# Kernel tuning notes

Measured on AMD Instinct MI355X. Metric: run time of the kernel, lower is better.

## Reference

```python
import jax, jax.numpy as jnp
import numpy as np
from jax import lax

B, T, D, H, V = 64, 512, 256, 1024, 32000


def setup_inputs() -> dict:
    key = jax.random.key(0)
    kx, kw, ku, kd = jax.random.split(key, 4)
    s_in = 1.0 / np.sqrt(D)
    s_h = 1.0 / np.sqrt(H)
    return {
        "x": jax.random.normal(kx, (B, T, D), dtype=jnp.float32),
        "W": jax.random.normal(kw, (D, H), dtype=jnp.float32) * s_in,
        "U": jax.random.normal(ku, (H, H), dtype=jnp.float32) * s_h,
        "b": jnp.zeros((H,), dtype=jnp.float32),
        "Wd": jax.random.normal(kd, (H, V), dtype=jnp.float32) * s_h,
        "bd": jnp.zeros((V,), dtype=jnp.float32),
    }


def reference(x, W, U, b, Wd, bd):
    # Precompute input projection for all timesteps: [B,T,H]
    xW = jnp.einsum("btd,dh->bth", x, W) + b

    def step(h, xw_t):
        # SimpleRNNCell: h_t = tanh(x_t W + b + h_{t-1} U)
        h_new = jnp.tanh(xw_t + h @ U)
        return h_new, None

    h0 = jnp.zeros((x.shape[0], U.shape[0]), dtype=x.dtype)
    hT, _ = lax.scan(step, h0, jnp.swapaxes(xW, 0, 1))  # scan over T

    logits = hT @ Wd + bd  # [B, V]
    return jax.nn.softmax(logits, axis=-1)
```

## Files before the change

### kernel.cpp

```cpp
#include <hip/hip_runtime.h>
#include <math.h>

#define CB 64
#define CT 512
#define CD 256
#define CH 1024
#define CV 32000

#define XS_STRIDE 280
#define WL_STRIDE 284
#define HR_ROW 1280

#define FLAG_STRIDE 32

typedef float f32x4 __attribute__((ext_vector_type(4)));

__device__ __forceinline__ unsigned ld_flag(const unsigned* p) {
  unsigned v;
  asm volatile("global_load_dword %0, %1, off sc0 sc1\n\ts_waitcnt vmcnt(0)"
               : "=v"(v) : "v"(p) : "memory");
  return v;
}
__device__ __forceinline__ void st_flag(unsigned* p, unsigned v) {
  asm volatile("global_store_dword %0, %1, off sc0 sc1" :: "v"(p), "v"(v) : "memory");
}
__device__ __forceinline__ void st_h4(float* p, f32x4 v) {
  asm volatile("global_store_dwordx4 %0, %1, off sc0 sc1" :: "v"(p), "v"(v) : "memory");
}
__device__ __forceinline__ void ld4_h(const float* p0, const float* p1,
                                      const float* p2, const float* p3,
                                      f32x4& a0, f32x4& a1, f32x4& a2, f32x4& a3) {
  asm volatile(
    "global_load_dwordx4 %0, %4, off sc0 sc1\n\t"
    "global_load_dwordx4 %1, %5, off sc0 sc1\n\t"
    "global_load_dwordx4 %2, %6, off sc0 sc1\n\t"
    "global_load_dwordx4 %3, %7, off sc0 sc1\n\t"
    "s_waitcnt vmcnt(0)"
    : "=&v"(a0), "=&v"(a1), "=&v"(a2), "=&v"(a3)
    : "v"(p0), "v"(p1), "v"(p2), "v"(p3)
    : "memory");
}

__device__ __forceinline__ void grid_barrier_fenced(unsigned* gbar, int bid, unsigned target) {
  __syncthreads();
  const int w = threadIdx.x >> 6, lane = threadIdx.x & 63;
  if (threadIdx.x == 0)
    __hip_atomic_store(gbar + (size_t)bid * FLAG_STRIDE, target,
                       __ATOMIC_RELEASE, __HIP_MEMORY_SCOPE_AGENT);
  if (w < 4) {
    const unsigned* f = gbar + (size_t)(w * 64 + lane) * FLAG_STRIDE;
    int spin = 0;
    unsigned v;
    do {
      v = __hip_atomic_load(f, __ATOMIC_RELAXED, __HIP_MEMORY_SCOPE_AGENT);
    } while (__any((int)(v < target)) && ++spin < (1 << 25));
  }
  __threadfence();
  __syncthreads();
}

extern "C" __global__ void __launch_bounds__(512, 1)
rnn_scan_kernel(const float* __restrict__ x, const float* __restrict__ W,
                const float* __restrict__ U, const float* __restrict__ bb,
                float* __restrict__ hbuf, float* __restrict__ xwbuf,
                unsigned* __restrict__ gbar, unsigned* __restrict__ sbar, int Tc)
{
  __shared__ float sA[18432];
  __shared__ float sB[18432];
  __shared__ float red[8][8][40];

  const int tid  = threadIdx.x;
  const int bid  = blockIdx.x;
  const int w    = tid >> 6;
  const int lane = tid & 63;

  const int xg = bid >> 5;
  const int sl = bid & 31;
  const int c0 = sl << 5;
  unsigned* myflag = sbar + (size_t)(xg * 32 + sl) * FLAG_STRIDE;
  const unsigned* fbase = sbar + (size_t)(xg * 32) * FLAG_STRIDE;

  const int r    = bid >> 6;
  const int q    = bid & 63;
  const int tsub = q >> 4, acg = q & 15;
  const int a_tw = w >> 1, a_jh = w & 1;
  const int a_kg = lane >> 5;
  const int a_pi = (lane >> 3) & 3;
  const int a_pj = lane & 7;
  const int a_jl = a_jh * 32 + a_pj * 4;
  const int a_jglob = acg * 64 + a_jl;
  float4 a_bias = *(const float4*)(bb + a_jglob);

  const int kg  = lane >> 3;
  const int ccg = lane & 7;
  const int kc  = w * 8 + kg;
  const int jb  = c0 + ccg * 4;

  f32x4 ureg[16];
  #pragma unroll
  for (int k = 0; k < 16; ++k)
    ureg[k] = *(const f32x4*)(U + (size_t)(kc * 16 + k) * CH + jb);

  const int nchunk = CT / Tc;
  const int tquarter = Tc >> 2;
  unsigned gep = 0;

  for (int chunk = 0; chunk < nchunk; ++chunk) {
    __syncthreads();
    for (int f = tid; f < 4096; f += 512) {
      int kk = f >> 4, seg = f & 15;
      float4 v = *(const float4*)(W + (size_t)kk * CH + acg * 64 + seg * 4);
      float* wrow = sB + (size_t)(seg * 4) * WL_STRIDE + kk + (seg & 7) * 4;
      wrow[0 * WL_STRIDE] = v.x;
      wrow[1 * WL_STRIDE] = v.y;
      wrow[2 * WL_STRIDE] = v.z;
      wrow[3 * WL_STRIDE] = v.w;
    }

    for (int tb = 0; tb < tquarter; tb += 4) {
      int nt = tquarter - tb; if (nt > 4) nt = 4;
      __syncthreads();
      for (int f = tid; f < nt * 1024; f += 512) {
        int tw = f >> 10, rem = f & 1023;
        int row = rem >> 6, col = (rem & 63) * 4;
        int t = chunk * Tc + tsub * tquarter + tb + tw;
        float4 v = *(const float4*)(x + ((size_t)(r * 16 + row) * CT + t) * CD + col);
        *(float4*)(sA + (size_t)(tw * 16 + row) * XS_STRIDE + col + ((row >> 2) & 3) * 8) = v;
      }
      __syncthreads();
      if (a_tw < nt) {
        int tloc = tsub * tquarter + tb + a_tw;
        float acc[4][4];
        #pragma unroll
        for (int i2 = 0; i2 < 4; ++i2)
          #pragma unroll
          for (int j2 = 0; j2 < 4; ++j2) acc[i2][j2] = 0.f;
        const float* xbase = sA + (size_t)(a_tw * 16 + a_pi * 4) * XS_STRIDE + a_kg * 128 + a_pi * 8;
        const float* wbase = sB + (size_t)a_jl * WL_STRIDE + a_kg * 128 + a_pj * 4;
        #pragma unroll 2
        for (int u = 0; u < 128; u += 4) {
          float4 ha[4], wb[4];
          #pragma unroll
          for (int di = 0; di < 4; ++di) ha[di] = *(const float4*)(xbase + (size_t)di * XS_STRIDE + u);
          #pragma unroll
          for (int dj = 0; dj < 4; ++dj) wb[dj] = *(const float4*)(wbase + (size_t)dj * WL_STRIDE + u);
          #pragma unroll
          for (int di = 0; di < 4; ++di)
            #pragma unroll
            for (int dj = 0; dj < 4; ++dj)
              acc[di][dj] += ha[di].x * wb[dj].x + ha[di].y * wb[dj].y
                           + ha[di].z * wb[dj].z + ha[di].w * wb[dj].w;
        }
        #pragma unroll
        for (int di = 0; di < 4; ++di)
          #pragma unroll
          for (int dj = 0; dj < 4; ++dj)
            acc[di][dj] += __shfl_xor(acc[di][dj], 32, 64);
        if (a_kg == 0) {
          size_t obase = (size_t)tloc * (CB * CH) + (size_t)(r * 16 + a_pi * 4) * CH + a_jglob;
          #pragma unroll
          for (int di = 0; di < 4; ++di) {
            float4 o;
            o.x = acc[di][0] + a_bias.x;
            o.y = acc[di][1] + a_bias.y;
            o.z = acc[di][2] + a_bias.z;
            o.w = acc[di][3] + a_bias.w;
            *(float4*)(xwbuf + obase + (size_t)di * CH) = o;
          }
        }
      }
      __syncthreads();
    }

    grid_barrier_fenced(gbar, bid, ++gep);

    for (int tc = 0; tc < Tc; ++tc) {
      const int g = chunk * Tc + tc;
      const float* hb_r = hbuf + (size_t)(g & 1) * (CB * CH);
      float*       hb_w = hbuf + (size_t)((g & 1) ^ 1) * (CB * CH);

      f32x4 zxw;
      if (w == 0) {
        zxw = *(const f32x4*)(xwbuf + (size_t)tc * (CB * CH)
                              + (size_t)(xg * 8 + (lane >> 3)) * CH + c0 + (lane & 7) * 4);
      }

      if (g > 0) {
        if (w == 0) {
          const unsigned* f = fbase + (size_t)(lane & 31) * FLAG_STRIDE;
          int spin = 0;
          unsigned v;
          do { v = ld_flag(f); } while (__any((int)(v < (unsigned)g)) && ++spin < (1 << 26));
        }
        __syncthreads();

        {
          const float* hr = hb_r + (size_t)(xg << 3) * CH;
          const int i0 = tid, i1 = tid + 512, i2 = tid + 1024, i3 = tid + 1536;
          const float* p0 = hr + ((size_t)(i0 >> 8) << 10) + ((i0 & 255) << 2);
          const float* p1 = hr + ((size_t)(i1 >> 8) << 10) + ((i1 & 255) << 2);
          const float* p2 = hr + ((size_t)(i2 >> 8) << 10) + ((i2 & 255) << 2);
          const float* p3 = hr + ((size_t)(i3 >> 8) << 10) + ((i3 & 255) << 2);
          f32x4 a0, a1, a2, a3;
          ld4_h(p0, p1, p2, p3, a0, a1, a2, a3);
          *(f32x4*)(sA + (i0 >> 8) * HR_ROW + ((i0 & 255) >> 2) * 20 + (i0 & 3) * 4) = a0;
          *(f32x4*)(sA + (i1 >> 8) * HR_ROW + ((i1 & 255) >> 2) * 20 + (i1 & 3) * 4) = a1;
          *(f32x4*)(sA + (i2 >> 8) * HR_ROW + ((i2 & 255) >> 2) * 20 + (i2 & 3) * 4) = a2;
          *(f32x4*)(sA + (i3 >> 8) * HR_ROW + ((i3 & 255) >> 2) * 20 + (i3 & 3) * 4) = a3;
        }
        __syncthreads();

        {
          const float* hbase = sA + kc * 20;
          f32x4 acc[8];
          #pragma unroll
          for (int di = 0; di < 8; ++di) acc[di] = (f32x4){0.f, 0.f, 0.f, 0.f};
          #pragma unroll
          for (int us = 0; us < 4; ++us) {
            const int u = us * 4;
            const f32x4 u0 = ureg[u + 0], u1 = ureg[u + 1], u2 = ureg[u + 2], u3 = ureg[u + 3];
            #pragma unroll
            for (int di = 0; di < 8; ++di) {
              const f32x4 hv = *(const f32x4*)(hbase + di * HR_ROW + u);
              acc[di] += hv.x * u0 + hv.y * u1 + hv.z * u2 + hv.w * u3;
            }
          }
          #pragma unroll
          for (int di = 0; di < 8; ++di) {
            #pragma unroll
            for (int m = 8; m < 64; m <<= 1) {
              acc[di].x += __shfl_xor(acc[di].x, m, 64);
              acc[di].y += __shfl_xor(acc[di].y, m, 64);
              acc[di].z += __shfl_xor(acc[di].z, m, 64);
              acc[di].w += __shfl_xor(acc[di].w, m, 64);
            }
          }
          if (kg == 0) {
            #pragma unroll
            for (int di = 0; di < 8; ++di)
              *(f32x4*)&red[w][di][ccg * 4] = acc[di];
          }
        }
        __syncthreads();
      }

      if (w == 0) {
        const int i = lane >> 3, j4 = lane & 7;
        f32x4 z = zxw;
        if (g > 0) {
          #pragma unroll
          for (int ww = 0; ww < 8; ++ww) {
            const f32x4 rv = *(const f32x4*)&red[ww][i][j4 * 4];
            z += rv;
          }
        }
        f32x4 o;
        o.x = tanhf(z.x); o.y = tanhf(z.y); o.z = tanhf(z.z); o.w = tanhf(z.w);
        st_h4(hb_w + (size_t)(xg * 8 + i) * CH + c0 + j4 * 4, o);
        asm volatile("s_waitcnt vmcnt(0)" ::: "memory");
        if (lane == 0) st_flag(myflag, (unsigned)(g + 1));
      }
    }

    if (chunk + 1 < nchunk) grid_barrier_fenced(gbar, bid, ++gep);
  }
}

extern "C" __global__ void __launch_bounds__(64, 1)
logits_kernel(const float* __restrict__ hfin, const float* __restrict__ Wd,
              const float* __restrict__ bd, float* __restrict__ out)
{
  __shared__ float al[64][68];
  __shared__ float wl[64][68];
  const int n0 = blockIdx.x * 64;
  const int lane = threadIdx.x;
  const int pi = lane >> 3, pj = lane & 7;
  float acc[8][8];
  #pragma unroll
  for (int a = 0; a < 8; ++a)
    #pragma unroll
    for (int bq = 0; bq < 8; ++bq) acc[a][bq] = 0.f;

  for (int k0 = 0; k0 < CH; k0 += 64) {
    __syncthreads();
    #pragma unroll
    for (int p = 0; p < 16; ++p) {
      int row = p * 4 + (lane >> 4);
      int seg = lane & 15;
      float4 v = *(const float4*)(hfin + (size_t)row * CH + k0 + seg * 4);
      al[seg * 4 + 0][row] = v.x;
      al[seg * 4 + 1][row] = v.y;
      al[seg * 4 + 2][row] = v.z;
      al[seg * 4 + 3][row] = v.w;
    }
    #pragma unroll
    for (int p = 0; p < 16; ++p) {
      int f = p * 64 + lane;
      int kk = f >> 4, seg = f & 15;
      *(float4*)&wl[kk][seg * 4] = *(const float4*)(Wd + (size_t)(k0 + kk) * CV + n0 + seg * 4);
    }
    __syncthreads();
    #pragma unroll 2
    for (int kk = 0; kk < 64; ++kk) {
      float av[8], bv[8];
      *(float4*)&av[0] = *(const float4*)&al[kk][pi * 8];
      *(float4*)&av[4] = *(const float4*)&al[kk][pi * 8 + 4];
      *(float4*)&bv[0] = *(const float4*)&wl[kk][pj * 8];
      *(float4*)&bv[4] = *(const float4*)&wl[kk][pj * 8 + 4];
      #pragma unroll
      for (int a = 0; a < 8; ++a)
        #pragma unroll
        for (int bq = 0; bq < 8; ++bq)
          acc[a][bq] += av[a] * bv[bq];
    }
  }
  float bdv[8];
  *(float4*)&bdv[0] = *(const float4*)(bd + n0 + pj * 8);
  *(float4*)&bdv[4] = *(const float4*)(bd + n0 + pj * 8 + 4);
  #pragma unroll
  for (int a = 0; a < 8; ++a) {
    int row = pi * 8 + a;
    float4 o0, o1;
    o0.x = acc[a][0] + bdv[0]; o0.y = acc[a][1] + bdv[1];
    o0.z = acc[a][2] + bdv[2]; o0.w = acc[a][3] + bdv[3];
    o1.x = acc[a][4] + bdv[4]; o1.y = acc[a][5] + bdv[5];
    o1.z = acc[a][6] + bdv[6]; o1.w = acc[a][7] + bdv[7];
    *(float4*)(out + (size_t)row * CV + n0 + pj * 8) = o0;
    *(float4*)(out + (size_t)row * CV + n0 + pj * 8 + 4) = o1;
  }
}

extern "C" __global__ void __launch_bounds__(256)
softmax_kernel(float* __restrict__ out)
{
  __shared__ float red[256];
  const int row = blockIdx.x;
  const int tid = threadIdx.x;
  float* p = out + (size_t)row * CV;
  float m = -3.4e38f;
  for (int i = tid; i < CV; i += 256) m = fmaxf(m, p[i]);
  red[tid] = m;
  __syncthreads();
  for (int s = 128; s > 0; s >>= 1) {
    if (tid < s) red[tid] = fmaxf(red[tid], red[tid + s]);
    __syncthreads();
  }
  m = red[0];
  __syncthreads();
  float sum = 0.f;
  for (int i = tid; i < CV; i += 256) {
    float e = expf(p[i] - m);
    p[i] = e;
    sum += e;
  }
  red[tid] = sum;
  __syncthreads();
  for (int s = 128; s > 0; s >>= 1) {
    if (tid < s) red[tid] = red[tid] + red[tid + s];
    __syncthreads();
  }
  float inv = 1.f / red[0];
  for (int i = tid; i < CV; i += 256) p[i] *= inv;
}

extern "C" __global__ void init_ws(unsigned* p) {
  p[(size_t)blockIdx.x * 1024 + threadIdx.x] = 0u;
}

extern "C" void kernel_launch(void* const* d_in, const int* in_sizes, int n_in,
                              void* d_out, int out_size, void* d_ws, size_t ws_size,
                              hipStream_t stream) {
  const float* x  = (const float*)d_in[0];
  const float* W  = (const float*)d_in[1];
  const float* U  = (const float*)d_in[2];
  const float* bb = (const float*)d_in[3];
  const float* Wd = (const float*)d_in[4];
  const float* bd = (const float*)d_in[5];
  float* out = (float*)d_out;

  char* ws = (char*)d_ws;
  unsigned* gbar = (unsigned*)ws;
  unsigned* sbar = (unsigned*)(ws + 32768);
  float* hbuf  = (float*)(ws + 65536);
  float* xwbuf = (float*)(ws + 65536 + (size_t)2 * CB * CH * sizeof(float));

  const int cands[7] = {512, 256, 128, 64, 32, 16, 8};
  int Tc = 4;
  for (int ci = 0; ci < 7; ++ci) {
    size_t need = 65536 + (size_t)2 * CB * CH * 4 + (size_t)cands[ci] * CB * CH * 4;
    if (need <= ws_size) { Tc = cands[ci]; break; }
  }

  hipLaunchKernelGGL(init_ws, dim3(16), dim3(1024), 0, stream, (unsigned*)ws);

  void* args[9];
  args[0] = (void*)&x;     args[1] = (void*)&W;     args[2] = (void*)&U;
  args[3] = (void*)&bb;    args[4] = (void*)&hbuf;  args[5] = (void*)&xwbuf;
  args[6] = (void*)&gbar;  args[7] = (void*)&sbar;  args[8] = (void*)&Tc;
  hipLaunchCooperativeKernel((void*)rnn_scan_kernel, dim3(256), dim3(512), args, 0, stream);

  hipLaunchKernelGGL(logits_kernel, dim3(CV / 64), dim3(64), 0, stream, hbuf, Wd, bd, out);
  hipLaunchKernelGGL(softmax_kernel, dim3(CB), dim3(256), 0, stream, out);
}
```

Before: 3.996 ms.

## Replace per-block step flags with tagged value-plus-step pairs in hidden state

Each hidden-state element is now stored together with its timestep tag as an 8-byte pair, so consumers poll the data itself instead of spinning on 32 producer flags and then loading h. This removes the separate flag store/load round trip, the vmcnt wait before the flag store and one block barrier per step. The tanh/store work is spread across four waves instead of one. In exchange, the hidden buffer doubles in size, every load carries tag words, and init_ws must zero a larger region. A separate final-h buffer is written at the last step for the logits kernel.

```diff
diff --git a/kernel.cpp b/kernel.cpp
--- a/kernel.cpp
+++ b/kernel.cpp
@@ -14,31 +14,14 @@
 #define FLAG_STRIDE 32
 
 typedef float f32x4 __attribute__((ext_vector_type(4)));
-
-__device__ __forceinline__ unsigned ld_flag(const unsigned* p) {
-  unsigned v;
-  asm volatile("global_load_dword %0, %1, off sc0 sc1\n\ts_waitcnt vmcnt(0)"
-               : "=v"(v) : "v"(p) : "memory");
-  return v;
-}
-__device__ __forceinline__ void st_flag(unsigned* p, unsigned v) {
-  asm volatile("global_store_dword %0, %1, off sc0 sc1" :: "v"(p), "v"(v) : "memory");
-}
-__device__ __forceinline__ void st_h4(float* p, f32x4 v) {
-  asm volatile("global_store_dwordx4 %0, %1, off sc0 sc1" :: "v"(p), "v"(v) : "memory");
-}
-__device__ __forceinline__ void ld4_h(const float* p0, const float* p1,
-                                      const float* p2, const float* p3,
-                                      f32x4& a0, f32x4& a1, f32x4& a2, f32x4& a3) {
-  asm volatile(
-    "global_load_dwordx4 %0, %4, off sc0 sc1\n\t"
-    "global_load_dwordx4 %1, %5, off sc0 sc1\n\t"
-    "global_load_dwordx4 %2, %6, off sc0 sc1\n\t"
-    "global_load_dwordx4 %3, %7, off sc0 sc1\n\t"
-    "s_waitcnt vmcnt(0)"
-    : "=&v"(a0), "=&v"(a1), "=&v"(a2), "=&v"(a3)
-    : "v"(p0), "v"(p1), "v"(p2), "v"(p3)
-    : "memory");
+typedef unsigned uint32x2 __attribute__((ext_vector_type(2)));
+typedef unsigned uint32x4 __attribute__((ext_vector_type(4)));
+
+__device__ __forceinline__ void st_pair(uint2* p, float v, unsigned tag) {
+  uint32x2 d;
+  d.x = __float_as_uint(v);
+  d.y = tag;
+  asm volatile("global_store_dwordx2 %0, %1, off sc0 sc1" :: "v"(p), "v"(d) : "memory");
 }
 
 __device__ __forceinline__ void grid_barrier_fenced(unsigned* gbar, int bid, unsigned target) {
@@ -62,8 +45,8 @@
 extern "C" __global__ void __launch_bounds__(512, 1)
 rnn_scan_kernel(const float* __restrict__ x, const float* __restrict__ W,
                 const float* __restrict__ U, const float* __restrict__ bb,
-                float* __restrict__ hbuf, float* __restrict__ xwbuf,
-                unsigned* __restrict__ gbar, unsigned* __restrict__ sbar, int Tc)
+                uint2* __restrict__ hpair, float* __restrict__ hfin,
+                float* __restrict__ xwbuf, unsigned* __restrict__ gbar, int Tc)
 {
   __shared__ float sA[18432];
   __shared__ float sB[18432];
@@ -77,8 +60,6 @@
   const int xg = bid >> 5;
   const int sl = bid & 31;
   const int c0 = sl << 5;
-  unsigned* myflag = sbar + (size_t)(xg * 32 + sl) * FLAG_STRIDE;
-  const unsigned* fbase = sbar + (size_t)(xg * 32) * FLAG_STRIDE;
 
   const int r    = bid >> 6;
   const int q    = bid & 63;
@@ -95,6 +76,9 @@
   const int ccg = lane & 7;
   const int kc  = w * 8 + kg;
   const int jb  = c0 + ccg * 4;
+
+  const int crow = tid >> 5;
+  const int ccol = tid & 31;
 
   f32x4 ureg[16];
   #pragma unroll
@@ -176,37 +160,52 @@
 
     for (int tc = 0; tc < Tc; ++tc) {
       const int g = chunk * Tc + tc;
-      const float* hb_r = hbuf + (size_t)(g & 1) * (CB * CH);
-      float*       hb_w = hbuf + (size_t)((g & 1) ^ 1) * (CB * CH);
-
-      f32x4 zxw;
-      if (w == 0) {
-        zxw = *(const f32x4*)(xwbuf + (size_t)tc * (CB * CH)
-                              + (size_t)(xg * 8 + (lane >> 3)) * CH + c0 + (lane & 7) * 4);
-      }
+      const uint2* hp_r = hpair + (size_t)(g & 1) * (CB * CH);
+      uint2*       hp_w = hpair + (size_t)((g & 1) ^ 1) * (CB * CH);
+
+      float zxw = 0.f;
+      if (w < 4)
+        zxw = xwbuf[(size_t)tc * (CB * CH) + (size_t)(xg * 8 + crow) * CH + c0 + ccol];
 
       if (g > 0) {
-        if (w == 0) {
-          const unsigned* f = fbase + (size_t)(lane & 31) * FLAG_STRIDE;
+        {
+          const uint2* pb = hp_r + (((size_t)(xg * 8 + w)) << 10) + lane * 16;
+          const unsigned tag = (unsigned)g;
+          uint32x4 q0, q1, q2, q3, q4, q5, q6, q7;
           int spin = 0;
-          unsigned v;
-          do { v = ld_flag(f); } while (__any((int)(v < (unsigned)g)) && ++spin < (1 << 26));
-        }
-        __syncthreads();
-
-        {
-          const float* hr = hb_r + (size_t)(xg << 3) * CH;
-          const int i0 = tid, i1 = tid + 512, i2 = tid + 1024, i3 = tid + 1536;
-          const float* p0 = hr + ((size_t)(i0 >> 8) << 10) + ((i0 & 255) << 2);
-          const float* p1 = hr + ((size_t)(i1 >> 8) << 10) + ((i1 & 255) << 2);
-          const float* p2 = hr + ((size_t)(i2 >> 8) << 10) + ((i2 & 255) << 2);
-          const float* p3 = hr + ((size_t)(i3 >> 8) << 10) + ((i3 & 255) << 2);
-          f32x4 a0, a1, a2, a3;
-          ld4_h(p0, p1, p2, p3, a0, a1, a2, a3);
-          *(f32x4*)(sA + (i0 >> 8) * HR_ROW + ((i0 & 255) >> 2) * 20 + (i0 & 3) * 4) = a0;
-          *(f32x4*)(sA + (i1 >> 8) * HR_ROW + ((i1 & 255) >> 2) * 20 + (i1 & 3) * 4) = a1;
-          *(f32x4*)(sA + (i2 >> 8) * HR_ROW + ((i2 & 255) >> 2) * 20 + (i2 & 3) * 4) = a2;
-          *(f32x4*)(sA + (i3 >> 8) * HR_ROW + ((i3 & 255) >> 2) * 20 + (i3 & 3) * 4) = a3;
+          bool ok;
+          do {
+            asm volatile(
+              "global_load_dwordx4 %0, %8, off sc0 sc1\n\t"
+              "global_load_dwordx4 %1, %8, off offset:16 sc0 sc1\n\t"
+              "global_load_dwordx4 %2, %8, off offset:32 sc0 sc1\n\t"
+              "global_load_dwordx4 %3, %8, off offset:48 sc0 sc1\n\t"
+              "global_load_dwordx4 %4, %8, off offset:64 sc0 sc1\n\t"
+              "global_load_dwordx4 %5, %8, off offset:80 sc0 sc1\n\t"
+              "global_load_dwordx4 %6, %8, off offset:96 sc0 sc1\n\t"
+              "global_load_dwordx4 %7, %8, off offset:112 sc0 sc1\n\t"
+              "s_waitcnt vmcnt(0)"
+              : "=&v"(q0), "=&v"(q1), "=&v"(q2), "=&v"(q3),
+                "=&v"(q4), "=&v"(q5), "=&v"(q6), "=&v"(q7)
+              : "v"(pb) : "memory");
+            ok = (q0.y == tag) & (q0.w == tag) & (q1.y == tag) & (q1.w == tag)
+               & (q2.y == tag) & (q2.w == tag) & (q3.y == tag) & (q3.w == tag)
+               & (q4.y == tag) & (q4.w == tag) & (q5.y == tag) & (q5.w == tag)
+               & (q6.y == tag) & (q6.w == tag) & (q7.y == tag) & (q7.w == tag);
+          } while (!ok && ++spin < (1 << 24));
+          float* dst = sA + (size_t)w * HR_ROW + lane * 20;
+          f32x4 f0 = { __uint_as_float(q0.x), __uint_as_float(q0.z),
+                       __uint_as_float(q1.x), __uint_as_float(q1.z) };
+          f32x4 f1 = { __uint_as_float(q2.x), __uint_as_float(q2.z),
+                       __uint_as_float(q3.x), __uint_as_float(q3.z) };
+          f32x4 f2 = { __uint_as_float(q4.x), __uint_as_float(q4.z),
+                       __uint_as_float(q5.x), __uint_as_float(q5.z) };
+          f32x4 f3 = { __uint_as_float(q6.x), __uint_as_float(q6.z),
+                       __uint_as_float(q7.x), __uint_as_float(q7.z) };
+          *(f32x4*)(dst + 0)  = f0;
+          *(f32x4*)(dst + 4)  = f1;
+          *(f32x4*)(dst + 8)  = f2;
+          *(f32x4*)(dst + 12) = f3;
         }
         __syncthreads();
 
@@ -244,21 +243,16 @@
         __syncthreads();
       }
 
-      if (w == 0) {
-        const int i = lane >> 3, j4 = lane & 7;
-        f32x4 z = zxw;
+      if (w < 4) {
+        float z = zxw;
         if (g > 0) {
           #pragma unroll
-          for (int ww = 0; ww < 8; ++ww) {
-            const f32x4 rv = *(const f32x4*)&red[ww][i][j4 * 4];
-            z += rv;
-          }
-        }
-        f32x4 o;
-        o.x = tanhf(z.x); o.y = tanhf(z.y); o.z = tanhf(z.z); o.w = tanhf(z.w);
-        st_h4(hb_w + (size_t)(xg * 8 + i) * CH + c0 + j4 * 4, o);
-        asm volatile("s_waitcnt vmcnt(0)" ::: "memory");
-        if (lane == 0) st_flag(myflag, (unsigned)(g + 1));
+          for (int ww = 0; ww < 8; ++ww) z += red[ww][crow][ccol];
+        }
+        float o = tanhf(z);
+        st_pair(hp_w + (((size_t)(xg * 8 + crow)) << 10) + c0 + ccol, o, (unsigned)(g + 1));
+        if (g == CT - 1)
+          hfin[(size_t)(xg * 8 + crow) * CH + c0 + ccol] = o;
       }
     }
 
@@ -380,25 +374,26 @@
 
   char* ws = (char*)d_ws;
   unsigned* gbar = (unsigned*)ws;
-  unsigned* sbar = (unsigned*)(ws + 32768);
-  float* hbuf  = (float*)(ws + 65536);
-  float* xwbuf = (float*)(ws + 65536 + (size_t)2 * CB * CH * sizeof(float));
-
+  uint2* hpair = (uint2*)(ws + 32768);
+  float* hfin  = (float*)(ws + 32768 + 1048576);
+  float* xwbuf = (float*)(ws + 32768 + 1048576 + 262144);
+
+  const size_t fixed = 32768 + 1048576 + 262144;
   const int cands[7] = {512, 256, 128, 64, 32, 16, 8};
   int Tc = 4;
   for (int ci = 0; ci < 7; ++ci) {
-    size_t need = 65536 + (size_t)2 * CB * CH * 4 + (size_t)cands[ci] * CB * CH * 4;
+    size_t need = fixed + (size_t)cands[ci] * CB * CH * 4;
     if (need <= ws_size) { Tc = cands[ci]; break; }
   }
 
-  hipLaunchKernelGGL(init_ws, dim3(16), dim3(1024), 0, stream, (unsigned*)ws);
+  hipLaunchKernelGGL(init_ws, dim3(264), dim3(1024), 0, stream, (unsigned*)ws);
 
   void* args[9];
   args[0] = (void*)&x;     args[1] = (void*)&W;     args[2] = (void*)&U;
-  args[3] = (void*)&bb;    args[4] = (void*)&hbuf;  args[5] = (void*)&xwbuf;
-  args[6] = (void*)&gbar;  args[7] = (void*)&sbar;  args[8] = (void*)&Tc;
+  args[3] = (void*)&bb;    args[4] = (void*)&hpair; args[5] = (void*)&hfin;
+  args[6] = (void*)&xwbuf; args[7] = (void*)&gbar;  args[8] = (void*)&Tc;
   hipLaunchCooperativeKernel((void*)rnn_scan_kernel, dim3(256), dim3(512), args, 0, stream);
 
-  hipLaunchKernelGGL(logits_kernel, dim3(CV / 64), dim3(64), 0, stream, hbuf, Wd, bd, out);
+  hipLaunchKernelGGL(logits_kernel, dim3(CV / 64), dim3(64), 0, stream, hfin, Wd, bd, out);
   hipLaunchKernelGGL(softmax_kernel, dim3(CB), dim3(256), 0, stream, out);
 }
```

Result: slower. 6.601 ms (+65.2%).

## Stage h per-wave into LDS and overlap loads with partial matvec, dropping a barrier

Applied to the files above, without the earlier changes.

Each wave now loads exactly the slice of h it consumes (its own k-range) into LDS. That lets it skip the block-wide __syncthreads between staging and compute, and it splits the four loads so the first half of the U-matvec starts while the second half is still in flight. Flag polling moves from wave 0 to wave 1, and the LDS row stride is padded from 1280 to 1288. The aim is to shorten the per-timestep critical path of the serial recurrence, at the cost of hand-placed waitcnt and sched barriers that must stay correct.

```diff
diff --git a/kernel.cpp b/kernel.cpp
--- a/kernel.cpp
+++ b/kernel.cpp
@@ -9,7 +9,7 @@
 
 #define XS_STRIDE 280
 #define WL_STRIDE 284
-#define HR_ROW 1280
+#define HR_ROW 1288
 
 #define FLAG_STRIDE 32
 
@@ -26,19 +26,6 @@
 }
 __device__ __forceinline__ void st_h4(float* p, f32x4 v) {
   asm volatile("global_store_dwordx4 %0, %1, off sc0 sc1" :: "v"(p), "v"(v) : "memory");
-}
-__device__ __forceinline__ void ld4_h(const float* p0, const float* p1,
-                                      const float* p2, const float* p3,
-                                      f32x4& a0, f32x4& a1, f32x4& a2, f32x4& a3) {
-  asm volatile(
-    "global_load_dwordx4 %0, %4, off sc0 sc1\n\t"
-    "global_load_dwordx4 %1, %5, off sc0 sc1\n\t"
-    "global_load_dwordx4 %2, %6, off sc0 sc1\n\t"
-    "global_load_dwordx4 %3, %7, off sc0 sc1\n\t"
-    "s_waitcnt vmcnt(0)"
-    : "=&v"(a0), "=&v"(a1), "=&v"(a2), "=&v"(a3)
-    : "v"(p0), "v"(p1), "v"(p2), "v"(p3)
-    : "memory");
 }
 
 __device__ __forceinline__ void grid_barrier_fenced(unsigned* gbar, int bid, unsigned target) {
@@ -95,6 +82,9 @@
   const int ccg = lane & 7;
   const int kc  = w * 8 + kg;
   const int jb  = c0 + ccg * 4;
+
+  const int s_row = lane >> 3;
+  const int s_k8  = lane & 7;
 
   f32x4 ureg[16];
   #pragma unroll
@@ -186,7 +176,7 @@
       }
 
       if (g > 0) {
-        if (w == 0) {
+        if (w == 1) {
           const unsigned* f = fbase + (size_t)(lane & 31) * FLAG_STRIDE;
           int spin = 0;
           unsigned v;
@@ -194,29 +184,30 @@
         }
         __syncthreads();
 
+        f32x4 acc[8];
+        #pragma unroll
+        for (int di = 0; di < 8; ++di) acc[di] = (f32x4){0.f, 0.f, 0.f, 0.f};
         {
-          const float* hr = hb_r + (size_t)(xg << 3) * CH;
-          const int i0 = tid, i1 = tid + 512, i2 = tid + 1024, i3 = tid + 1536;
-          const float* p0 = hr + ((size_t)(i0 >> 8) << 10) + ((i0 & 255) << 2);
-          const float* p1 = hr + ((size_t)(i1 >> 8) << 10) + ((i1 & 255) << 2);
-          const float* p2 = hr + ((size_t)(i2 >> 8) << 10) + ((i2 & 255) << 2);
-          const float* p3 = hr + ((size_t)(i3 >> 8) << 10) + ((i3 & 255) << 2);
+          const float* pb = hb_r + (size_t)(xg * 8 + s_row) * CH + w * 128 + s_k8 * 16;
           f32x4 a0, a1, a2, a3;
-          ld4_h(p0, p1, p2, p3, a0, a1, a2, a3);
-          *(f32x4*)(sA + (i0 >> 8) * HR_ROW + ((i0 & 255) >> 2) * 20 + (i0 & 3) * 4) = a0;
-          *(f32x4*)(sA + (i1 >> 8) * HR_ROW + ((i1 & 255) >> 2) * 20 + (i1 & 3) * 4) = a1;
-          *(f32x4*)(sA + (i2 >> 8) * HR_ROW + ((i2 & 255) >> 2) * 20 + (i2 & 3) * 4) = a2;
-          *(f32x4*)(sA + (i3 >> 8) * HR_ROW + ((i3 & 255) >> 2) * 20 + (i3 & 3) * 4) = a3;
-        }
-        __syncthreads();
-
-        {
+          asm volatile(
+            "global_load_dwordx4 %0, %4, off sc0 sc1\n\t"
+            "global_load_dwordx4 %1, %4, off offset:16 sc0 sc1\n\t"
+            "global_load_dwordx4 %2, %4, off offset:32 sc0 sc1\n\t"
+            "global_load_dwordx4 %3, %4, off offset:48 sc0 sc1"
+            : "=&v"(a0), "=&v"(a1), "=&v"(a2), "=&v"(a3)
+            : "v"(pb) : "memory");
+          float* dst = sA + (size_t)s_row * HR_ROW + (w * 8 + s_k8) * 20;
           const float* hbase = sA + kc * 20;
-          f32x4 acc[8];
-          #pragma unroll
-          for (int di = 0; di < 8; ++di) acc[di] = (f32x4){0.f, 0.f, 0.f, 0.f};
-          #pragma unroll
-          for (int us = 0; us < 4; ++us) {
+
+          asm volatile("s_waitcnt vmcnt(2)" ::: "memory");
+          __builtin_amdgcn_sched_barrier(0);
+          *(f32x4*)(dst + 0) = a0;
+          *(f32x4*)(dst + 4) = a1;
+          asm volatile("s_waitcnt lgkmcnt(0)" ::: "memory");
+          __builtin_amdgcn_sched_barrier(0);
+          #pragma unroll
+          for (int us = 0; us < 2; ++us) {
             const int u = us * 4;
             const f32x4 u0 = ureg[u + 0], u1 = ureg[u + 1], u2 = ureg[u + 2], u3 = ureg[u + 3];
             #pragma unroll
@@ -225,21 +216,39 @@
               acc[di] += hv.x * u0 + hv.y * u1 + hv.z * u2 + hv.w * u3;
             }
           }
-          #pragma unroll
-          for (int di = 0; di < 8; ++di) {
+
+          asm volatile("s_waitcnt vmcnt(0)" ::: "memory");
+          __builtin_amdgcn_sched_barrier(0);
+          *(f32x4*)(dst + 8)  = a2;
+          *(f32x4*)(dst + 12) = a3;
+          asm volatile("s_waitcnt lgkmcnt(0)" ::: "memory");
+          __builtin_amdgcn_sched_barrier(0);
+          #pragma unroll
+          for (int us = 2; us < 4; ++us) {
+            const int u = us * 4;
+            const f32x4 u0 = ureg[u + 0], u1 = ureg[u + 1], u2 = ureg[u + 2], u3 = ureg[u + 3];
             #pragma unroll
-            for (int m = 8; m < 64; m <<= 1) {
-              acc[di].x += __shfl_xor(acc[di].x, m, 64);
-              acc[di].y += __shfl_xor(acc[di].y, m, 64);
-              acc[di].z += __shfl_xor(acc[di].z, m, 64);
-              acc[di].w += __shfl_xor(acc[di].w, m, 64);
+            for (int di = 0; di < 8; ++di) {
+              const f32x4 hv = *(const f32x4*)(hbase + di * HR_ROW + u);
+              acc[di] += hv.x * u0 + hv.y * u1 + hv.z * u2 + hv.w * u3;
             }
           }
-          if (kg == 0) {
-            #pragma unroll
-            for (int di = 0; di < 8; ++di)
-              *(f32x4*)&red[w][di][ccg * 4] = acc[di];
+        }
+
+        #pragma unroll
+        for (int di = 0; di < 8; ++di) {
+          #pragma unroll
+          for (int m = 8; m < 64; m <<= 1) {
+            acc[di].x += __shfl_xor(acc[di].x, m, 64);
+            acc[di].y += __shfl_xor(acc[di].y, m, 64);
+            acc[di].z += __shfl_xor(acc[di].z, m, 64);
+            acc[di].w += __shfl_xor(acc[di].w, m, 64);
           }
+        }
+        if (kg == 0) {
+          #pragma unroll
+          for (int di = 0; di < 8; ++di)
+            *(f32x4*)&red[w][di][ccg * 4] = acc[di];
         }
         __syncthreads();
       }
```

Result: slower. 4.115 ms (+3.0%).
